# Optimization experiments

Measured on AMD Instinct MI355X. Metric: run time of the kernel, lower is better.

## Reference

```python
import jax, jax.numpy as jnp
import numpy as np

D_K = 128
NEG_BIG = 1e32  # matches torch's -1e+32 additive mask (finite in fp32)


def setup_inputs() -> dict:
    key = jax.random.key(0)
    kq, kk, kv, kqp, kkp = jax.random.split(key, 5)
    B, M, N, d_k, d_v = 8, 2048, 2048, D_K, 128
    return {
        "queries": jax.random.normal(kq, (B, M, d_k), dtype=jnp.float32),
        "keys": jax.random.normal(kk, (B, N, d_k), dtype=jnp.float32),
        "values": jax.random.normal(kv, (B, N, d_v), dtype=jnp.float32),
        "q_pres": jax.random.randint(kqp, (B, M), 0, 2, dtype=jnp.int32),
        "k_pres": jax.random.randint(kkp, (B, N), 0, 2, dtype=jnp.int32),
    }


def reference(queries, keys, values, q_pres, k_pres):
    # routing: [B, M, N] = Q K^T with multiplicative presence masking
    routing = jnp.einsum("bmd,bnd->bmn", queries, keys)
    qp = q_pres.astype(jnp.float32)  # [B, M]
    kp = k_pres.astype(jnp.float32)  # [B, N]
    routing = routing * qp[:, :, None]
    routing = routing * kp[:, None, :]
    # additive -1e32 mask for absent keys, then scaled softmax over N
    routing = routing - (1.0 - kp[:, None, :]) * NEG_BIG
    routing = jax.nn.softmax(routing / np.sqrt(D_K).astype(np.float32), axis=-1)
    return jnp.einsum("bmn,bnv->bmv", routing, values)
```

## Files before the change

kernel.cpp:

```cpp
#include <hip/hip_runtime.h>
#include <cstddef>
#include <cstdint>

#define SEQ_M 2048
#define SEQ_N 2048
#define DKV 128
#define BN 64
#define NCH 4
#define CHKEYS (SEQ_N / NCH)
#define NTILES 32
#define NREC (NCH * 8 * NTILES)

typedef _Float16 f16x8 __attribute__((ext_vector_type(8)));
typedef _Float16 f16x4 __attribute__((ext_vector_type(4)));
typedef float f32x4 __attribute__((ext_vector_type(4)));

#if defined(__has_builtin)
#if __has_builtin(__builtin_amdgcn_exp2f)
#define EXP2F(x) __builtin_amdgcn_exp2f(x)
#else
#define EXP2F(x) exp2f(x)
#endif
#else
#define EXP2F(x) exp2f(x)
#endif

#define SM_SCALE 0.12751745f
#define BIG_NEG 1.2751745e31f

#define KH_OFF 0
#define VH_OFF (256 * 8192)
#define P16_OFF (2 * 256 * 8192)
#define ML_BYTE_OFF ((size_t)(P16_OFF + (size_t)NREC * 8192) * 2)
#define WS_NEED (ML_BYTE_OFF + (size_t)NREC * 128 * 4)

#define AS1 __attribute__((address_space(1)))
#define AS3 __attribute__((address_space(3)))

__device__ __forceinline__ void copy16(const void* g, void* lds_base,
                                       void* lds_lane) {
#if defined(__has_builtin) && __has_builtin(__builtin_amdgcn_global_load_lds)
  __builtin_amdgcn_global_load_lds((const AS1 void*)g, (AS3 void*)lds_base, 16,
                                   0, 0);
  (void)lds_lane;
#else
  *(f16x8*)lds_lane = *(const f16x8*)g;
#endif
}

__global__ __launch_bounds__(256) void prep(const float* __restrict__ Kg,
                                            const float* __restrict__ Vg,
                                            _Float16* __restrict__ Kh,
                                            _Float16* __restrict__ Vh) {
  const int b = blockIdx.x & 7;
  const int nt = blockIdx.x >> 3;
  const int t = threadIdx.x;
  const float* Kb = Kg + ((size_t)b * SEQ_N + nt * 64) * DKV;
  const float* Vb = Vg + ((size_t)b * SEQ_N + nt * 64) * DKV;
  _Float16* Kt_ = Kh + (size_t)(b * NTILES + nt) * 8192;
  _Float16* Vt_ = Vh + (size_t)(b * NTILES + nt) * 8192;
#pragma unroll
  for (int i = 0; i < 4; ++i) {
    const int idx = i * 256 + t;
    const int c = idx & 15, key = idx >> 4;
    const float* src = Kb + key * DKV + c * 8;
    const float4 a0 = *(const float4*)src;
    const float4 a1 = *(const float4*)(src + 4);
    f16x8 h;
    h[0] = (_Float16)a0.x; h[1] = (_Float16)a0.y;
    h[2] = (_Float16)a0.z; h[3] = (_Float16)a0.w;
    h[4] = (_Float16)a1.x; h[5] = (_Float16)a1.y;
    h[6] = (_Float16)a1.z; h[7] = (_Float16)a1.w;
    *(f16x8*)&Kt_[c * 512 + key * 8] = h;
  }
#pragma unroll
  for (int i = 0; i < 4; ++i) {
    const int idx = i * 256 + t;
    const int vcol = idx & 127, g = idx >> 7;
    f16x8 h;
#pragma unroll
    for (int j = 0; j < 8; ++j)
      h[j] = (_Float16)Vb[(size_t)(g * 8 + j) * DKV + vcol];
    *(f16x8*)&Vt_[vcol * 64 + ((g ^ (vcol & 7)) * 8)] = h;
  }
}

__global__ __launch_bounds__(256, 4) void attn_core2(
    const _Float16* __restrict__ Kh, const _Float16* __restrict__ Vh,
    const float* __restrict__ Qg, const int* __restrict__ QPg,
    const int* __restrict__ KPg, _Float16* __restrict__ P16,
    float* __restrict__ ML) {
  __shared__ _Float16 smem[16384];
  _Float16* const Kt = smem;
  _Float16* const Vt = smem + 8192;

  const int tid = threadIdx.x;
  const int w = tid >> 6;
  const int lane = tid & 63;
  const int q16 = lane & 15;
  const int quad = lane >> 4;
  _Float16* const Pl = smem + w * 1152;

  const int b = blockIdx.x & 7;
  const int rest = blockIdx.x >> 3;
  const int mt = rest & 31;
  const int chk = rest >> 5;

  const int qrow = mt * 64 + w * 16 + q16;
  const float* qptr = Qg + ((size_t)b * SEQ_M + qrow) * DKV;
  const float qs = QPg[b * SEQ_M + qrow] ? 1.0f : 0.0f;
  f16x8 qf[4];
#pragma unroll
  for (int kc = 0; kc < 4; ++kc) {
    const float4 a0 = *(const float4*)(qptr + kc * 32 + quad * 8);
    const float4 a1 = *(const float4*)(qptr + kc * 32 + quad * 8 + 4);
    f16x8 h;
    h[0] = (_Float16)(a0.x * qs); h[1] = (_Float16)(a0.y * qs);
    h[2] = (_Float16)(a0.z * qs); h[3] = (_Float16)(a0.w * qs);
    h[4] = (_Float16)(a1.x * qs); h[5] = (_Float16)(a1.y * qs);
    h[6] = (_Float16)(a1.z * qs); h[7] = (_Float16)(a1.w * qs);
    qf[kc] = h;
  }

  f32x4 o[8];
#pragma unroll
  for (int vt = 0; vt < 8; ++vt) o[vt] = (f32x4){0.f, 0.f, 0.f, 0.f};
  float m_run = -3.0e38f;
  float l_run = 0.f;

  for (int ti = 0; ti < CHKEYS / BN; ++ti) {
    const int nt = chk * 8 + ti;
    __syncthreads();

    {
      const char* gsrc =
          (w < 2) ? (const char*)(Kh + (size_t)(b * NTILES + nt) * 8192) +
                        w * 8192
                  : (const char*)(Vh + (size_t)(b * NTILES + nt) * 8192) +
                        (w - 2) * 8192;
      char* ldst = (w < 2) ? (char*)Kt + w * 8192 : (char*)Vt + (w - 2) * 8192;
#pragma unroll
      for (int r = 0; r < 8; ++r)
        copy16(gsrc + r * 1024 + lane * 16, ldst + r * 1024,
               ldst + r * 1024 + lane * 16);
    }
    const unsigned long long kmask =
        __ballot(KPg[(size_t)b * SEQ_N + nt * 64 + lane] != 0);
    __syncthreads();

    f32x4 st[4];
#pragma unroll
    for (int t = 0; t < 4; ++t) st[t] = (f32x4){0.f, 0.f, 0.f, 0.f};
#pragma unroll
    for (int kc = 0; kc < 4; ++kc) {
      const f16x8 qv = qf[kc];
#pragma unroll
      for (int t = 0; t < 4; ++t) {
        const f16x8 kf =
            *(const f16x8*)&Kt[((kc * 4 + quad) * 64 + t * 16 + q16) * 8];
        st[t] = __builtin_amdgcn_mfma_f32_16x16x32_f16(kf, qv, st[t], 0, 0, 0);
      }
    }

    float s2[16];
    float mx = -3.0e38f;
#pragma unroll
    for (int t = 0; t < 4; ++t)
#pragma unroll
      for (int r = 0; r < 4; ++r) {
        const int key = t * 16 + quad * 4 + r;
        const float v =
            ((kmask >> key) & 1ull) ? st[t][r] * SM_SCALE : -BIG_NEG;
        s2[t * 4 + r] = v;
        mx = fmaxf(mx, v);
      }
    mx = fmaxf(mx, __shfl_xor(mx, 16));
    mx = fmaxf(mx, __shfl_xor(mx, 32));
    const float mnew = fmaxf(m_run, mx);
    const float alpha = EXP2F(m_run - mnew);
    m_run = mnew;

    float p[16];
    float psum = 0.f;
#pragma unroll
    for (int i = 0; i < 16; ++i) {
      p[i] = EXP2F(s2[i] - mnew);
      psum += p[i];
    }
    psum += __shfl_xor(psum, 16);
    psum += __shfl_xor(psum, 32);
    l_run = l_run * alpha + psum;

    float arow[4];
#pragma unroll
    for (int r = 0; r < 4; ++r) arow[r] = __shfl(alpha, quad * 4 + r);
#pragma unroll
    for (int vt = 0; vt < 8; ++vt) {
      o[vt][0] *= arow[0]; o[vt][1] *= arow[1];
      o[vt][2] *= arow[2]; o[vt][3] *= arow[3];
    }

    __syncthreads();

#pragma unroll
    for (int t = 0; t < 4; ++t) {
      f16x4 pw;
      pw[0] = (_Float16)p[t * 4 + 0];
      pw[1] = (_Float16)p[t * 4 + 1];
      pw[2] = (_Float16)p[t * 4 + 2];
      pw[3] = (_Float16)p[t * 4 + 3];
      *(f16x4*)&Pl[q16 * 72 + t * 16 + quad * 4] = pw;
    }
    const f16x8 pf0 = *(const f16x8*)&Pl[q16 * 72 + quad * 8];
    const f16x8 pf1 = *(const f16x8*)&Pl[q16 * 72 + 32 + quad * 8];
#pragma unroll
    for (int vt = 0; vt < 8; ++vt) {
      const int vcol = vt * 16 + q16;
      const f16x8 v0 =
          *(const f16x8*)&Vt[vcol * 64 + ((quad ^ (vcol & 7)) * 8)];
      o[vt] = __builtin_amdgcn_mfma_f32_16x16x32_f16(pf0, v0, o[vt], 0, 0, 0);
      const f16x8 v1 =
          *(const f16x8*)&Vt[vcol * 64 + (((quad + 4) ^ (vcol & 7)) * 8)];
      o[vt] = __builtin_amdgcn_mfma_f32_16x16x32_f16(pf1, v1, o[vt], 0, 0, 0);
    }
  }

  float linv[4];
#pragma unroll
  for (int r = 0; r < 4; ++r) linv[r] = 1.0f / __shfl(l_run, quad * 4 + r);
  const int rec = (chk * 8 + b) * 32 + mt;
  _Float16* ob = P16 + (size_t)rec * 8192 + (size_t)(w * 16) * 128;
#pragma unroll
  for (int vt = 0; vt < 8; ++vt)
#pragma unroll
    for (int r = 0; r < 4; ++r)
      ob[(quad * 4 + r) * 128 + vt * 16 + q16] =
          (_Float16)(o[vt][r] * linv[r]);
  if (quad == 0) {
    float* ml = ML + (size_t)rec * 128;
    ml[w * 16 + q16] = m_run;
    ml[64 + w * 16 + q16] = l_run;
  }
}

__global__ __launch_bounds__(256) void attn_combine(
    const _Float16* __restrict__ P16, const float* __restrict__ ML,
    float* __restrict__ Og) {
  const int t = threadIdx.x;
  const int b = blockIdx.x & 7;
  const int mt = blockIdx.x >> 3;
  __shared__ float msh[NCH][64];
  __shared__ float lsh[NCH][64];
  {
    const int c = t >> 6, row = t & 63;
    const float* ml = ML + (size_t)(((c * 8 + b) * 32) + mt) * 128;
    msh[c][row] = ml[row];
    lsh[c][row] = ml[64 + row];
  }
  __syncthreads();
  const int colh = (t & 31) * 4;
  const int rg = t >> 5;
  const _Float16* recO[NCH];
#pragma unroll
  for (int c = 0; c < NCH; ++c)
    recO[c] = P16 + (size_t)(((c * 8 + b) * 32) + mt) * 8192;
  float* outb = Og + ((size_t)b * SEQ_M + mt * 64) * DKV;
#pragma unroll
  for (int rr = 0; rr < 8; ++rr) {
    const int row = rr * 8 + rg;
    float M = -3.0e38f;
#pragma unroll
    for (int c = 0; c < NCH; ++c) M = fmaxf(M, msh[c][row]);
    float wgt[NCH];
    float lt = 0.f;
#pragma unroll
    for (int c = 0; c < NCH; ++c) {
      wgt[c] = EXP2F(msh[c][row] - M) * lsh[c][row];
      lt += wgt[c];
    }
    const float inv = 1.0f / lt;
    f32x4 acc = (f32x4){0.f, 0.f, 0.f, 0.f};
#pragma unroll
    for (int c = 0; c < NCH; ++c) {
      const f16x4 v = *(const f16x4*)(recO[c] + (size_t)row * 128 + colh);
      acc[0] += wgt[c] * (float)v[0]; acc[1] += wgt[c] * (float)v[1];
      acc[2] += wgt[c] * (float)v[2]; acc[3] += wgt[c] * (float)v[3];
    }
    f32x4 r;
    r[0] = acc[0] * inv; r[1] = acc[1] * inv;
    r[2] = acc[2] * inv; r[3] = acc[3] * inv;
    *(f32x4*)(outb + (size_t)row * DKV + colh) = r;
  }
}

__global__ __launch_bounds__(256) void attn_fallback(
    const float* __restrict__ Qg, const float* __restrict__ Kg,
    const float* __restrict__ Vg, const int* __restrict__ QPg,
    const int* __restrict__ KPg, float* __restrict__ Og) {
  __shared__ _Float16 smem[16 * 65 * 8 + 128 * 72];
  _Float16* const Kt = smem;
  _Float16* const Vt = smem + 16 * 65 * 8;
  const int tid = threadIdx.x;
  const int w = tid >> 6;
  const int lane = tid & 63;
  const int q16 = lane & 15;
  const int quad = lane >> 4;
  _Float16* const Pl = smem + w * (16 * 72);
  const int b = blockIdx.x & 7;
  const int mb = (blockIdx.x >> 3) * 64;
  const int qrow = mb + w * 16 + q16;
  const float* qptr = Qg + ((size_t)b * SEQ_M + qrow) * DKV;
  const float qs = QPg[b * SEQ_M + qrow] ? 1.0f : 0.0f;
  f16x8 qf[4];
#pragma unroll
  for (int kc = 0; kc < 4; ++kc) {
    const float4 a0 = *(const float4*)(qptr + kc * 32 + quad * 8);
    const float4 a1 = *(const float4*)(qptr + kc * 32 + quad * 8 + 4);
    f16x8 h;
    h[0] = (_Float16)(a0.x * qs); h[1] = (_Float16)(a0.y * qs);
    h[2] = (_Float16)(a0.z * qs); h[3] = (_Float16)(a0.w * qs);
    h[4] = (_Float16)(a1.x * qs); h[5] = (_Float16)(a1.y * qs);
    h[6] = (_Float16)(a1.z * qs); h[7] = (_Float16)(a1.w * qs);
    qf[kc] = h;
  }
  f32x4 o[8];
#pragma unroll
  for (int vt = 0; vt < 8; ++vt) o[vt] = (f32x4){0.f, 0.f, 0.f, 0.f};
  float m_run = -3.0e38f, l_run = 0.f;
  const int kn = tid >> 2, ks = (tid & 3) * 32;
  const int vg = tid >> 3, vk = (tid & 7) * 8;
  for (int n0 = 0; n0 < SEQ_N; n0 += BN) {
    __syncthreads();
    {
      const float* kp_ = Kg + ((size_t)b * SEQ_N + n0 + kn) * DKV + ks;
#pragma unroll
      for (int c2 = 0; c2 < 4; ++c2) {
        const float4 a0 = *(const float4*)(kp_ + c2 * 8);
        const float4 a1 = *(const float4*)(kp_ + c2 * 8 + 4);
        f16x8 h;
        h[0] = (_Float16)a0.x; h[1] = (_Float16)a0.y;
        h[2] = (_Float16)a0.z; h[3] = (_Float16)a0.w;
        h[4] = (_Float16)a1.x; h[5] = (_Float16)a1.y;
        h[6] = (_Float16)a1.z; h[7] = (_Float16)a1.w;
        *(f16x8*)&Kt[(((ks >> 3) + c2) * 65 + kn) * 8] = h;
      }
    }
    {
      const float* vp0 = Vg + ((size_t)b * SEQ_N + n0 + vk) * DKV + vg * 4;
      float4 vv[8];
#pragma unroll
      for (int j = 0; j < 8; ++j) vv[j] = *(const float4*)(vp0 + (size_t)j * DKV);
#pragma unroll
      for (int i = 0; i < 4; ++i) {
        f16x8 h;
#pragma unroll
        for (int j = 0; j < 8; ++j) h[j] = (_Float16)(((const float*)&vv[j])[i]);
        *(f16x8*)&Vt[(vg * 4 + i) * 72 + vk] = h;
      }
    }
    const unsigned long long kmask =
        __ballot(KPg[(size_t)b * SEQ_N + n0 + lane] != 0);
    __syncthreads();
    f32x4 st[4];
#pragma unroll
    for (int t = 0; t < 4; ++t) st[t] = (f32x4){0.f, 0.f, 0.f, 0.f};
#pragma unroll
    for (int kc = 0; kc < 4; ++kc) {
      const f16x8 qv = qf[kc];
#pragma unroll
      for (int t = 0; t < 4; ++t) {
        const f16x8 kf =
            *(const f16x8*)&Kt[((kc * 4 + quad) * 65 + t * 16 + q16) * 8];
        st[t] = __builtin_amdgcn_mfma_f32_16x16x32_f16(kf, qv, st[t], 0, 0, 0);
      }
    }
    float s2[16];
    float mx = -3.0e38f;
#pragma unroll
    for (int t = 0; t < 4; ++t)
#pragma unroll
      for (int r = 0; r < 4; ++r) {
        const int key = t * 16 + quad * 4 + r;
        const float v =
            ((kmask >> key) & 1ull) ? st[t][r] * SM_SCALE : -BIG_NEG;
        s2[t * 4 + r] = v;
        mx = fmaxf(mx, v);
      }
    mx = fmaxf(mx, __shfl_xor(mx, 16));
    mx = fmaxf(mx, __shfl_xor(mx, 32));
    const float mnew = fmaxf(m_run, mx);
    const float alpha = EXP2F(m_run - mnew);
    m_run = mnew;
    float p[16];
    float psum = 0.f;
#pragma unroll
    for (int i = 0; i < 16; ++i) {
      p[i] = EXP2F(s2[i] - mnew);
      psum += p[i];
    }
    psum += __shfl_xor(psum, 16);
    psum += __shfl_xor(psum, 32);
    l_run = l_run * alpha + psum;
    float arow[4];
#pragma unroll
    for (int r = 0; r < 4; ++r) arow[r] = __shfl(alpha, quad * 4 + r);
#pragma unroll
    for (int vt = 0; vt < 8; ++vt) {
      o[vt][0] *= arow[0]; o[vt][1] *= arow[1];
      o[vt][2] *= arow[2]; o[vt][3] *= arow[3];
    }
    __syncthreads();
#pragma unroll
    for (int t = 0; t < 4; ++t) {
      f16x4 pw;
      pw[0] = (_Float16)p[t * 4 + 0];
      pw[1] = (_Float16)p[t * 4 + 1];
      pw[2] = (_Float16)p[t * 4 + 2];
      pw[3] = (_Float16)p[t * 4 + 3];
      *(f16x4*)&Pl[q16 * 72 + t * 16 + quad * 4] = pw;
    }
    const f16x8 pf0 = *(const f16x8*)&Pl[q16 * 72 + quad * 8];
    const f16x8 pf1 = *(const f16x8*)&Pl[q16 * 72 + 32 + quad * 8];
#pragma unroll
    for (int vt = 0; vt < 8; ++vt) {
      const f16x8 v0 = *(const f16x8*)&Vt[(vt * 16 + q16) * 72 + quad * 8];
      o[vt] = __builtin_amdgcn_mfma_f32_16x16x32_f16(pf0, v0, o[vt], 0, 0, 0);
      const f16x8 v1 = *(const f16x8*)&Vt[(vt * 16 + q16) * 72 + 32 + quad * 8];
      o[vt] = __builtin_amdgcn_mfma_f32_16x16x32_f16(pf1, v1, o[vt], 0, 0, 0);
    }
  }
  float linv[4];
#pragma unroll
  for (int r = 0; r < 4; ++r) linv[r] = 1.0f / __shfl(l_run, quad * 4 + r);
  float* obase = Og + ((size_t)b * SEQ_M + mb + w * 16) * DKV;
#pragma unroll
  for (int vt = 0; vt < 8; ++vt)
#pragma unroll
    for (int r = 0; r < 4; ++r)
      obase[(size_t)(quad * 4 + r) * DKV + vt * 16 + q16] = o[vt][r] * linv[r];
}

extern "C" void kernel_launch(void* const* d_in, const int* in_sizes, int n_in,
                              void* d_out, int out_size, void* d_ws,
                              size_t ws_size, hipStream_t stream) {
  const float* Q = (const float*)d_in[0];
  const float* K = (const float*)d_in[1];
  const float* V = (const float*)d_in[2];
  const int* QP = (const int*)d_in[3];
  const int* KP = (const int*)d_in[4];
  float* O = (float*)d_out;
  if (ws_size >= WS_NEED) {
    _Float16* wsh = (_Float16*)d_ws;
    _Float16* Kh = wsh + KH_OFF;
    _Float16* Vh = wsh + VH_OFF;
    _Float16* P16 = wsh + P16_OFF;
    float* ML = (float*)((char*)d_ws + ML_BYTE_OFF);
    prep<<<dim3(256), dim3(256), 0, stream>>>(K, V, Kh, Vh);
    attn_core2<<<dim3(8 * NTILES * NCH), dim3(256), 0, stream>>>(
        Kh, Vh, Q, QP, KP, P16, ML);
    attn_combine<<<dim3(8 * NTILES), dim3(256), 0, stream>>>(P16, ML, O);
  } else {
    attn_fallback<<<dim3(8 * NTILES), dim3(256), 0, stream>>>(Q, K, V, QP, KP,
                                                              O);
  }
}
```

Before: 117.1 us.

## Double query tile per block to 128 rows with 512 threads sharing K/V tiles

The attention core now uses 512-thread blocks covering 128 query rows, so each K/V tile staged in LDS serves twice as many queries and the block count halves. The P staging buffer moves to its own LDS region, which removes one __syncthreads per key tile. The combine kernel is adjusted to the new record layout. LDS per block grows, which may lower occupancy, and the grid shrinks to 512 blocks.

New measurement: 114.0 us. 2.6% less time.

```diff
diff --git a/kernel.cpp b/kernel.cpp
--- a/kernel.cpp
+++ b/kernel.cpp
@@ -8,8 +8,9 @@
 #define BN 64
 #define NCH 4
 #define CHKEYS (SEQ_N / NCH)
-#define NTILES 32
-#define NREC (NCH * 8 * NTILES)
+#define NKT 32
+#define MT2 16
+#define NREC (NCH * 8 * MT2)
 
 typedef _Float16 f16x8 __attribute__((ext_vector_type(8)));
 typedef _Float16 f16x4 __attribute__((ext_vector_type(4)));
@@ -31,8 +32,8 @@
 #define KH_OFF 0
 #define VH_OFF (256 * 8192)
 #define P16_OFF (2 * 256 * 8192)
-#define ML_BYTE_OFF ((size_t)(P16_OFF + (size_t)NREC * 8192) * 2)
-#define WS_NEED (ML_BYTE_OFF + (size_t)NREC * 128 * 4)
+#define ML_BYTE_OFF ((size_t)(P16_OFF + (size_t)NREC * 16384) * 2)
+#define WS_NEED (ML_BYTE_OFF + (size_t)NREC * 256 * 4)
 
 #define AS1 __attribute__((address_space(1)))
 #define AS3 __attribute__((address_space(3)))
@@ -57,8 +58,8 @@
   const int t = threadIdx.x;
   const float* Kb = Kg + ((size_t)b * SEQ_N + nt * 64) * DKV;
   const float* Vb = Vg + ((size_t)b * SEQ_N + nt * 64) * DKV;
-  _Float16* Kt_ = Kh + (size_t)(b * NTILES + nt) * 8192;
-  _Float16* Vt_ = Vh + (size_t)(b * NTILES + nt) * 8192;
+  _Float16* Kt_ = Kh + (size_t)(b * NKT + nt) * 8192;
+  _Float16* Vt_ = Vh + (size_t)(b * NKT + nt) * 8192;
 #pragma unroll
   for (int i = 0; i < 4; ++i) {
     const int idx = i * 256 + t;
@@ -85,12 +86,12 @@
   }
 }
 
-__global__ __launch_bounds__(256, 4) void attn_core2(
+__global__ __launch_bounds__(512, 4) void attn_core3(
     const _Float16* __restrict__ Kh, const _Float16* __restrict__ Vh,
     const float* __restrict__ Qg, const int* __restrict__ QPg,
     const int* __restrict__ KPg, _Float16* __restrict__ P16,
     float* __restrict__ ML) {
-  __shared__ _Float16 smem[16384];
+  __shared__ _Float16 smem[16384 + 8 * 1152];
   _Float16* const Kt = smem;
   _Float16* const Vt = smem + 8192;
 
@@ -99,14 +100,14 @@
   const int lane = tid & 63;
   const int q16 = lane & 15;
   const int quad = lane >> 4;
-  _Float16* const Pl = smem + w * 1152;
+  _Float16* const Pl = smem + 16384 + w * 1152;
 
   const int b = blockIdx.x & 7;
   const int rest = blockIdx.x >> 3;
-  const int mt = rest & 31;
-  const int chk = rest >> 5;
-
-  const int qrow = mt * 64 + w * 16 + q16;
+  const int mt = rest & 15;
+  const int chk = rest >> 4;
+
+  const int qrow = mt * 128 + w * 16 + q16;
   const float* qptr = Qg + ((size_t)b * SEQ_M + qrow) * DKV;
   const float qs = QPg[b * SEQ_M + qrow] ? 1.0f : 0.0f;
   f16x8 qf[4];
@@ -134,13 +135,12 @@
 
     {
       const char* gsrc =
-          (w < 2) ? (const char*)(Kh + (size_t)(b * NTILES + nt) * 8192) +
-                        w * 8192
-                  : (const char*)(Vh + (size_t)(b * NTILES + nt) * 8192) +
-                        (w - 2) * 8192;
-      char* ldst = (w < 2) ? (char*)Kt + w * 8192 : (char*)Vt + (w - 2) * 8192;
-#pragma unroll
-      for (int r = 0; r < 8; ++r)
+          (w < 4) ? (const char*)(Kh + (size_t)(b * NKT + nt) * 8192) + w * 4096
+                  : (const char*)(Vh + (size_t)(b * NKT + nt) * 8192) +
+                        (w - 4) * 4096;
+      char* ldst = (w < 4) ? (char*)Kt + w * 4096 : (char*)Vt + (w - 4) * 4096;
+#pragma unroll
+      for (int r = 0; r < 4; ++r)
         copy16(gsrc + r * 1024 + lane * 16, ldst + r * 1024,
                ldst + r * 1024 + lane * 16);
     }
@@ -199,8 +199,6 @@
       o[vt][0] *= arow[0]; o[vt][1] *= arow[1];
       o[vt][2] *= arow[2]; o[vt][3] *= arow[3];
     }
-
-    __syncthreads();
 
 #pragma unroll
     for (int t = 0; t < 4; ++t) {
@@ -228,8 +226,8 @@
   float linv[4];
 #pragma unroll
   for (int r = 0; r < 4; ++r) linv[r] = 1.0f / __shfl(l_run, quad * 4 + r);
-  const int rec = (chk * 8 + b) * 32 + mt;
-  _Float16* ob = P16 + (size_t)rec * 8192 + (size_t)(w * 16) * 128;
+  const int rec = (chk * 8 + b) * MT2 + mt;
+  _Float16* ob = P16 + (size_t)rec * 16384 + (size_t)(w * 16) * 128;
 #pragma unroll
   for (int vt = 0; vt < 8; ++vt)
 #pragma unroll
@@ -237,25 +235,27 @@
       ob[(quad * 4 + r) * 128 + vt * 16 + q16] =
           (_Float16)(o[vt][r] * linv[r]);
   if (quad == 0) {
-    float* ml = ML + (size_t)rec * 128;
+    float* ml = ML + (size_t)rec * 256;
     ml[w * 16 + q16] = m_run;
-    ml[64 + w * 16 + q16] = l_run;
-  }
-}
-
-__global__ __launch_bounds__(256) void attn_combine(
+    ml[128 + w * 16 + q16] = l_run;
+  }
+}
+
+__global__ __launch_bounds__(256) void attn_combine2(
     const _Float16* __restrict__ P16, const float* __restrict__ ML,
     float* __restrict__ Og) {
   const int t = threadIdx.x;
   const int b = blockIdx.x & 7;
   const int mt = blockIdx.x >> 3;
-  __shared__ float msh[NCH][64];
-  __shared__ float lsh[NCH][64];
-  {
-    const int c = t >> 6, row = t & 63;
-    const float* ml = ML + (size_t)(((c * 8 + b) * 32) + mt) * 128;
+  __shared__ float msh[NCH][128];
+  __shared__ float lsh[NCH][128];
+#pragma unroll
+  for (int i = 0; i < 2; ++i) {
+    const int idx = i * 256 + t;
+    const int c = idx >> 7, row = idx & 127;
+    const float* ml = ML + (size_t)((c * 8 + b) * MT2 + mt) * 256;
     msh[c][row] = ml[row];
-    lsh[c][row] = ml[64 + row];
+    lsh[c][row] = ml[128 + row];
   }
   __syncthreads();
   const int colh = (t & 31) * 4;
@@ -263,10 +263,10 @@
   const _Float16* recO[NCH];
 #pragma unroll
   for (int c = 0; c < NCH; ++c)
-    recO[c] = P16 + (size_t)(((c * 8 + b) * 32) + mt) * 8192;
-  float* outb = Og + ((size_t)b * SEQ_M + mt * 64) * DKV;
-#pragma unroll
-  for (int rr = 0; rr < 8; ++rr) {
+    recO[c] = P16 + (size_t)((c * 8 + b) * MT2 + mt) * 16384;
+  float* outb = Og + ((size_t)b * SEQ_M + mt * 128) * DKV;
+#pragma unroll
+  for (int rr = 0; rr < 16; ++rr) {
     const int row = rr * 8 + rg;
     float M = -3.0e38f;
 #pragma unroll
@@ -456,11 +456,10 @@
     _Float16* P16 = wsh + P16_OFF;
     float* ML = (float*)((char*)d_ws + ML_BYTE_OFF);
     prep<<<dim3(256), dim3(256), 0, stream>>>(K, V, Kh, Vh);
-    attn_core2<<<dim3(8 * NTILES * NCH), dim3(256), 0, stream>>>(
+    attn_core3<<<dim3(8 * MT2 * NCH), dim3(512), 0, stream>>>(
         Kh, Vh, Q, QP, KP, P16, ML);
-    attn_combine<<<dim3(8 * NTILES), dim3(256), 0, stream>>>(P16, ML, O);
+    attn_combine2<<<dim3(8 * MT2), dim3(256), 0, stream>>>(P16, ML, O);
   } else {
-    attn_fallback<<<dim3(8 * NTILES), dim3(256), 0, stream>>>(Q, K, V, QP, KP,
-                                                              O);
-  }
-}
+    attn_fallback<<<dim3(8 * 32), dim3(256), 0, stream>>>(Q, K, V, QP, KP, O);
+  }
+}
```
